# Optimization experiments

Measured on AMD Instinct MI355X. Metric: run time of the kernel, lower is better.

## Reference

```python
import jax, jax.numpy as jnp
import numpy as np

N_HEADS = 16


def setup_inputs() -> dict:
    key = jax.random.key(0)
    ks = jax.random.split(key, 9)
    B, T, C, S = 32, 8, 1024, 4096
    w_scale = 1.0 / np.sqrt(C).astype(np.float32)
    return {
        "x": jax.random.normal(ks[0], (B, T, C), jnp.float32),
        "cache_k": jax.random.normal(ks[1], (B, S, C), jnp.float32),
        "cache_v": jax.random.normal(ks[2], (B, S, C), jnp.float32),
        "cache_len": jax.random.randint(ks[3], (B,), 0, S - T, jnp.int32),
        "wq": jax.random.normal(ks[4], (C, C), jnp.float32) * w_scale,
        "wk": jax.random.normal(ks[5], (C, C), jnp.float32) * w_scale,
        "wv": jax.random.normal(ks[6], (C, C), jnp.float32) * w_scale,
        "wo": jax.random.normal(ks[7], (C, C), jnp.float32) * w_scale,
        "bo": jnp.zeros((C,), jnp.float32),
    }


def reference(x, cache_k, cache_v, cache_len, wq, wk, wv, wo, bo):
    # Decode step with KV cache (use_cache=True, window_size=None, mask=None).
    B, T, C = x.shape
    S = cache_k.shape[1]  # max_seq_len (static pad; torch pads to max(cache_len))
    H = N_HEADS
    hd = C // H

    # Projections (torch Linear: y = x @ W^T)
    q = x @ wq.T
    k_new = x @ wk.T
    v_new = x @ wv.T

    # Ragged past-KV gather: zero-pad each row beyond its cache_len,
    # exactly like the per-batch loop + padded_k/padded_v in torch.
    pos = jnp.arange(S)
    past_mask = (pos[None, :] < cache_len[:, None])[..., None]  # (B, S, 1)
    past_k = jnp.where(past_mask, cache_k, 0.0)
    past_v = jnp.where(past_mask, cache_v, 0.0)

    k = jnp.concatenate([past_k, k_new], axis=1)  # (B, S+T, C)
    v = jnp.concatenate([past_v, v_new], axis=1)

    def to_heads(t):
        return t.reshape(B, t.shape[1], H, hd).transpose(0, 2, 1, 3)

    qh, kh, vh = to_heads(q), to_heads(k), to_heads(v)  # (B,H,*,hd)

    scores = jnp.einsum('bhqd,bhkd->bhqk', qh, kh) / np.sqrt(hd).astype(np.float32)

    # Torch only materializes keys up to max(cache_len); slots beyond that
    # do not exist there, so mask them out. Slots in [cache_len_b, max_cl)
    # are zero-padded keys (score 0, value 0) in torch -> kept as-is here.
    max_cl = jnp.max(cache_len)
    key_valid = jnp.concatenate([pos < max_cl, jnp.ones((T,), bool)])  # (S+T,)
    NEG = jnp.float32(-1e30)
    scores = jnp.where(key_valid[None, None, None, :], scores, NEG)

    attn = jax.nn.softmax(scores, axis=-1)
    out = jnp.einsum('bhqk,bhkd->bhqd', attn, vh)
    out = out.transpose(0, 2, 1, 3).reshape(B, T, C)
    return out @ wo.T + bo
```

## Files before the change

### kernel.cpp

```cpp
#include <hip/hip_runtime.h>

constexpr int Bn = 32, Tn = 8, Cn = 1024, Sn = 4096, Hn = 16, HDn = 64;
constexpr int CHUNK = 64, NCHUNK = 64;
constexpr int KSPLIT = 4;
constexpr float SCALE = 0.125f;

constexpr size_t PROJ_PART = (size_t)Bn * Tn * Cn;
constexpr size_t QP_OFF = 0;
constexpr size_t KP_OFF = QP_OFF + KSPLIT * PROJ_PART;
constexpr size_t VP_OFF = KP_OFF + KSPLIT * PROJ_PART;
constexpr size_t PACC_OFF = VP_OFF + KSPLIT * PROJ_PART;
constexpr size_t PACC_SZ = (size_t)NCHUNK * Bn * Hn * Tn * HDn;
constexpr size_t PL_OFF = PACC_OFF + PACC_SZ;
constexpr size_t PL_SZ = (size_t)NCHUNK * Bn * Hn * Tn;
constexpr size_t AW_OFF = PL_OFF + PL_SZ;
constexpr size_t AW_SZ = PROJ_PART;
constexpr size_t OP_OFF = AW_OFF + AW_SZ;
constexpr size_t OP_SZ = (size_t)KSPLIT * PROJ_PART;
constexpr size_t QR_OFF = OP_OFF + OP_SZ;
constexpr size_t KN_OFF = QR_OFF + PROJ_PART;
constexpr size_t VN_OFF = KN_OFF + PROJ_PART;

typedef __attribute__((address_space(3))) unsigned int lds_uint;
typedef const __attribute__((address_space(1))) unsigned int glb_uint;

__device__ __forceinline__ void gload_lds16(const float* g, float* l) {
    __builtin_amdgcn_global_load_lds((glb_uint*)g, (lds_uint*)l, 16, 0, 0);
}

__device__ __forceinline__ void gemm_body(const float* __restrict__ X,
                                          const float* __restrict__ W,
                                          float* __restrict__ Opart,
                                          int sigma, int jblk, int iblk) {
    __shared__ float wl[64][68];
    const int tid = threadIdx.x;
    const int c = tid & 15, a = tid >> 4;
    const int j0 = jblk * 64;
    const int ib = iblk * 64 + a * 4;
    const int k0 = sigma * 256;

    float acc[4][4];
#pragma unroll
    for (int ii = 0; ii < 4; ++ii)
#pragma unroll
        for (int jj = 0; jj < 4; ++jj) acc[ii][jj] = 0.f;

    for (int kt = 0; kt < 4; ++kt) {
        const int k1 = k0 + kt * 64;
#pragma unroll
        for (int stp = 0; stp < 4; ++stp) {
            int f4 = stp * 256 + tid;
            int jr = f4 >> 4, e4 = f4 & 15;
            float4 wv = *(const float4*)&W[(size_t)(j0 + jr) * Cn + k1 + e4 * 4];
            wl[e4 * 4 + 0][jr] = wv.x;
            wl[e4 * 4 + 1][jr] = wv.y;
            wl[e4 * 4 + 2][jr] = wv.z;
            wl[e4 * 4 + 3][jr] = wv.w;
        }
        __syncthreads();
#pragma unroll 4
        for (int k4 = 0; k4 < 16; ++k4) {
            float4 xv[4];
#pragma unroll
            for (int ii = 0; ii < 4; ++ii)
                xv[ii] = *(const float4*)&X[(size_t)(ib + ii) * Cn + k1 + k4 * 4];
#pragma unroll
            for (int kk = 0; kk < 4; ++kk) {
                float4 wv = *(const float4*)&wl[k4 * 4 + kk][c * 4];
#pragma unroll
                for (int ii = 0; ii < 4; ++ii) {
                    const float xs = (kk == 0) ? xv[ii].x : (kk == 1) ? xv[ii].y
                                   : (kk == 2) ? xv[ii].z : xv[ii].w;
                    acc[ii][0] += xs * wv.x;
                    acc[ii][1] += xs * wv.y;
                    acc[ii][2] += xs * wv.z;
                    acc[ii][3] += xs * wv.w;
                }
            }
        }
        __syncthreads();
    }
    float* op = Opart + (size_t)sigma * PROJ_PART;
#pragma unroll
    for (int ii = 0; ii < 4; ++ii) {
        float4 o = make_float4(acc[ii][0], acc[ii][1], acc[ii][2], acc[ii][3]);
        *(float4*)&op[(size_t)(ib + ii) * Cn + j0 + c * 4] = o;
    }
}

__global__ __launch_bounds__(256) void proj3_kernel(
    const float* __restrict__ X, const float* __restrict__ W0,
    const float* __restrict__ W1, const float* __restrict__ W2,
    float* __restrict__ O0, float* __restrict__ O1, float* __restrict__ O2) {
    const int z = blockIdx.z;
    const float* W = (z < 4) ? W0 : (z < 8 ? W1 : W2);
    float* O = (z < 4) ? O0 : (z < 8 ? O1 : O2);
    gemm_body(X, W, O, z & 3, blockIdx.x, blockIdx.y);
}

__global__ __launch_bounds__(256) void gemm1_kernel(
    const float* __restrict__ X, const float* __restrict__ W, float* __restrict__ O) {
    gemm_body(X, W, O, blockIdx.z, blockIdx.x, blockIdx.y);
}

__global__ __launch_bounds__(256) void prereduce_kernel(
    const float* __restrict__ qp, const float* __restrict__ kp,
    const float* __restrict__ vp, float* __restrict__ q,
    float* __restrict__ kn, float* __restrict__ vn) {
    const size_t i = ((size_t)blockIdx.x * 256 + threadIdx.x) * 4;
#define SUM4(P)                                                              \
    make_float4(                                                             \
        (*(const float4*)(P + i)).x + (*(const float4*)(P + PROJ_PART + i)).x + \
        (*(const float4*)(P + 2 * PROJ_PART + i)).x + (*(const float4*)(P + 3 * PROJ_PART + i)).x, \
        (*(const float4*)(P + i)).y + (*(const float4*)(P + PROJ_PART + i)).y + \
        (*(const float4*)(P + 2 * PROJ_PART + i)).y + (*(const float4*)(P + 3 * PROJ_PART + i)).y, \
        (*(const float4*)(P + i)).z + (*(const float4*)(P + PROJ_PART + i)).z + \
        (*(const float4*)(P + 2 * PROJ_PART + i)).z + (*(const float4*)(P + 3 * PROJ_PART + i)).z, \
        (*(const float4*)(P + i)).w + (*(const float4*)(P + PROJ_PART + i)).w + \
        (*(const float4*)(P + 2 * PROJ_PART + i)).w + (*(const float4*)(P + 3 * PROJ_PART + i)).w)
    float4 qv = SUM4(qp);
    qv.x *= SCALE; qv.y *= SCALE; qv.z *= SCALE; qv.w *= SCALE;
    *(float4*)&q[i] = qv;
    *(float4*)&kn[i] = SUM4(kp);
    *(float4*)&vn[i] = SUM4(vp);
#undef SUM4
}

__global__ __launch_bounds__(64) void attn_kernel(
    const float* __restrict__ q, const float* __restrict__ kn,
    const float* __restrict__ vn, const float* __restrict__ ck,
    const float* __restrict__ cv, const int* __restrict__ clen,
    float* __restrict__ pacc, float* __restrict__ pl) {
    const int h = blockIdx.x, cq = blockIdx.y, b = blockIdx.z;
    const int cl = clen[b];
    if (cq != 0 && cq * CHUNK >= cl) return;

    const int lane = threadIdx.x;
    const int rg = lane >> 4;
    const int slot = lane & 15;

    __shared__ float K_l[64][64];
    __shared__ float V_l[64][64];
    __shared__ float q_l[8][64];
    __shared__ float p_l[8][64];

    {
        const float* qb = q + (size_t)b * Tn * Cn + (size_t)h * HDn;
#pragma unroll
        for (int i = 0; i < 2; ++i) {
            const int row = i * 4 + rg;
            gload_lds16(qb + (size_t)row * Cn + slot * 4, &q_l[i * 4][0]);
        }
    }
    const size_t gb = ((size_t)b * Sn + (size_t)cq * CHUNK) * Cn + (size_t)h * HDn;
#pragma unroll
    for (int i = 0; i < 16; ++i) {
        const int row = i * 4 + rg;
        gload_lds16(ck + gb + (size_t)row * Cn + (slot ^ (row & 15)) * 4, &K_l[i * 4][0]);
    }
#pragma unroll
    for (int i = 0; i < 16; ++i) {
        const int row = i * 4 + rg;
        gload_lds16(cv + gb + (size_t)row * Cn + slot * 4, &V_l[i * 4][0]);
    }

    int mv = clen[lane & 31];
#pragma unroll
    for (int off = 16; off >= 1; off >>= 1) {
        int o = __shfl_xor(mv, off);
        mv = mv > o ? mv : o;
    }

    const int nv = min(max(cl - cq * CHUNK, 0), CHUNK);

    asm volatile("s_waitcnt vmcnt(0)" ::: "memory");
    __builtin_amdgcn_sched_barrier(0);

    float s[8];
#pragma unroll
    for (int t = 0; t < 8; ++t) s[t] = 0.f;
    const int swz = lane & 15;
#pragma unroll
    for (int dg = 0; dg < 16; ++dg) {
        const float4 kv = *(const float4*)&K_l[lane][(dg ^ swz) * 4];
#pragma unroll
        for (int t = 0; t < 8; ++t) {
            const float4 qv = *(const float4*)&q_l[t][dg * 4];
            s[t] += kv.x * qv.x + kv.y * qv.y + kv.z * qv.z + kv.w * qv.w;
        }
    }
    const bool val = lane < nv;
    float lden[8];
#pragma unroll
    for (int t = 0; t < 8; ++t) {
        const float p = val ? __expf(s[t]) : 0.f;
        lden[t] = p;
        p_l[t][lane] = p;
    }

    float av[8];
#pragma unroll
    for (int t = 0; t < 8; ++t) av[t] = 0.f;
#pragma unroll 4
    for (int r4 = 0; r4 < 16; ++r4) {
        float4 pt[8];
#pragma unroll
        for (int t = 0; t < 8; ++t) pt[t] = *(const float4*)&p_l[t][r4 * 4];
        const float v0 = V_l[r4 * 4 + 0][lane];
        const float v1 = V_l[r4 * 4 + 1][lane];
        const float v2 = V_l[r4 * 4 + 2][lane];
        const float v3 = V_l[r4 * 4 + 3][lane];
#pragma unroll
        for (int t = 0; t < 8; ++t)
            av[t] += pt[t].x * v0 + pt[t].y * v1 + pt[t].z * v2 + pt[t].w * v3;
    }

    if (cq == 0) {
        const int r = lane >> 3, dgrp = lane & 7;
        const float* kb = kn + ((size_t)b * Tn + r) * Cn + (size_t)h * HDn + dgrp * 8;
        const float4 ka = *(const float4*)(kb);
        const float4 kc = *(const float4*)(kb + 4);
        float sn[8];
#pragma unroll
        for (int t = 0; t < 8; ++t) {
            const float4 qa = *(const float4*)&q_l[t][dgrp * 8];
            const float4 qc = *(const float4*)&q_l[t][dgrp * 8 + 4];
            float v = ka.x * qa.x + ka.y * qa.y + ka.z * qa.z + ka.w * qa.w +
                      kc.x * qc.x + kc.y * qc.y + kc.z * qc.z + kc.w * qc.w;
            v += __shfl_xor(v, 1);
            v += __shfl_xor(v, 2);
            v += __shfl_xor(v, 4);
            sn[t] = v;
        }
        if (dgrp == 0) {
#pragma unroll
            for (int t = 0; t < 8; ++t) {
                const float p = __expf(sn[t]);
                p_l[t][r] = p;
                lden[t] += p;
            }
        }
        const float* vb2 = vn + (size_t)b * Tn * Cn + (size_t)h * HDn + lane;
#pragma unroll
        for (int r2 = 0; r2 < 8; ++r2) {
            const float v = vb2[(size_t)r2 * Cn];
#pragma unroll
            for (int t = 0; t < 8; ++t) av[t] += p_l[t][r2] * v;
        }
    }

#pragma unroll
    for (int t = 0; t < 8; ++t) {
        float v = lden[t];
#pragma unroll
        for (int off = 32; off >= 1; off >>= 1) v += __shfl_xor(v, off);
        lden[t] = v;
    }
    if (cq == 0) {
        const float pad = (float)(mv - cl);
#pragma unroll
        for (int t = 0; t < 8; ++t) lden[t] += pad;
    }

    const size_t obase = (size_t)((cq * Bn + b) * Hn + h);
#pragma unroll
    for (int t = 0; t < 8; ++t) pacc[obase * 512 + (size_t)t * 64 + lane] = av[t];
    if (lane == 0) {
#pragma unroll
        for (int t = 0; t < 8; ++t) pl[obase * 8 + t] = lden[t];
    }
}

__global__ __launch_bounds__(256) void attn_merge_kernel(
    const float* __restrict__ pacc, const float* __restrict__ pl,
    const int* __restrict__ clen, float* __restrict__ aw) {
    const int h = blockIdx.x, b = blockIdx.y;
    const int tid = threadIdx.x, wave = tid >> 6, lane = tid & 63;
    const int cl = clen[b];
    int nch = (cl + CHUNK - 1) / CHUNK;
    if (nch < 1) nch = 1;

    __shared__ float racc[4][8][64];
    __shared__ float rl[4][8];

    float acc[8], l[8];
#pragma unroll
    for (int t = 0; t < 8; ++t) { acc[t] = 0.f; l[t] = 0.f; }
    for (int c = wave; c < nch; c += 4) {
        const size_t base = (size_t)((c * Bn + b) * Hn + h);
#pragma unroll
        for (int t = 0; t < 8; ++t) acc[t] += pacc[base * 512 + t * 64 + lane];
#pragma unroll
        for (int t = 0; t < 8; ++t) l[t] += pl[base * 8 + t];
    }
#pragma unroll
    for (int t = 0; t < 8; ++t) racc[wave][t][lane] = acc[t];
    if (lane == 0) {
#pragma unroll
        for (int t = 0; t < 8; ++t) rl[wave][t] = l[t];
    }
    __syncthreads();
#pragma unroll
    for (int rep = 0; rep < 2; ++rep) {
        const int e = rep * 256 + tid;
        const int t = e >> 6, d = e & 63;
        const float a = racc[0][t][d] + racc[1][t][d] + racc[2][t][d] + racc[3][t][d];
        const float ll = rl[0][t] + rl[1][t] + rl[2][t] + rl[3][t];
        aw[(size_t)(b * Tn + t) * Cn + (size_t)h * HDn + d] = a / ll;
    }
}

__global__ __launch_bounds__(256) void bias_out_kernel(
    const float* __restrict__ opart, const float* __restrict__ bo, float* __restrict__ out) {
    const int f4 = blockIdx.x * 256 + threadIdx.x;
    const float4 a0 = *(const float4*)(opart + (size_t)f4 * 4);
    const float4 a1 = *(const float4*)(opart + PROJ_PART + (size_t)f4 * 4);
    const float4 a2 = *(const float4*)(opart + 2 * PROJ_PART + (size_t)f4 * 4);
    const float4 a3 = *(const float4*)(opart + 3 * PROJ_PART + (size_t)f4 * 4);
    const float4 bv = *(const float4*)&bo[(f4 & 255) * 4];
    float4 o = make_float4(a0.x + a1.x + a2.x + a3.x + bv.x,
                           a0.y + a1.y + a2.y + a3.y + bv.y,
                           a0.z + a1.z + a2.z + a3.z + bv.z,
                           a0.w + a1.w + a2.w + a3.w + bv.w);
    *(float4*)&out[(size_t)f4 * 4] = o;
}

extern "C" void kernel_launch(void* const* d_in, const int* in_sizes, int n_in,
                              void* d_out, int out_size, void* d_ws, size_t ws_size,
                              hipStream_t stream) {
    const float* x  = (const float*)d_in[0];
    const float* ck = (const float*)d_in[1];
    const float* cv = (const float*)d_in[2];
    const int*   cl = (const int*)d_in[3];
    const float* wq = (const float*)d_in[4];
    const float* wk = (const float*)d_in[5];
    const float* wv = (const float*)d_in[6];
    const float* wo = (const float*)d_in[7];
    const float* bo = (const float*)d_in[8];
    float* out = (float*)d_out;
    float* ws = (float*)d_ws;

    float* qpart = ws + QP_OFF;
    float* kpart = ws + KP_OFF;
    float* vpart = ws + VP_OFF;
    float* pacc  = ws + PACC_OFF;
    float* pl    = ws + PL_OFF;
    float* aw    = ws + AW_OFF;
    float* opart = ws + OP_OFF;
    float* qr    = ws + QR_OFF;
    float* knew  = ws + KN_OFF;
    float* vnew  = ws + VN_OFF;

    proj3_kernel<<<dim3(16, 4, 12), dim3(256), 0, stream>>>(x, wq, wk, wv, qpart, kpart, vpart);
    prereduce_kernel<<<dim3(256), dim3(256), 0, stream>>>(qpart, kpart, vpart, qr, knew, vnew);
    attn_kernel<<<dim3(Hn, NCHUNK, Bn), dim3(64), 0, stream>>>(qr, knew, vnew, ck, cv, cl, pacc, pl);
    attn_merge_kernel<<<dim3(Hn, Bn), dim3(256), 0, stream>>>(pacc, pl, cl, aw);
    gemm1_kernel<<<dim3(16, 4, KSPLIT), dim3(256), 0, stream>>>(aw, wo, opart);
    bias_out_kernel<<<dim3(256), dim3(256), 0, stream>>>(opart, bo, out);
}
```

Before: 223.8 us.

## Make attention kernel persistent and stream V rows through registers

The attention kernel becomes a persistent grid of 2048 single-wave blocks that grid-stride over (batch, chunk, head) work items instead of launching one block per item. V is no longer staged in LDS; it is loaded into registers in four 16-row groups, with each next group's loads issued before the P·V accumulation of the current group so they overlap. Q is read directly from global memory (cache) instead of LDS, and a partial vmcnt wait lets the QK step start once K has landed. This cuts LDS use and per-block launch cost and hides V latency, at the cost of more registers, repeated global Q reads, and possible load imbalance from the fixed strided work split.

Measured after the change: 320.8 us. 1.43x slower.

```diff
diff --git a/kernel.cpp b/kernel.cpp
--- a/kernel.cpp
+++ b/kernel.cpp
@@ -2,6 +2,7 @@
 
 constexpr int Bn = 32, Tn = 8, Cn = 1024, Sn = 4096, Hn = 16, HDn = 64;
 constexpr int CHUNK = 64, NCHUNK = 64;
+constexpr int PERSIST = 2048;
 constexpr int KSPLIT = 4;
 constexpr float SCALE = 0.125f;
 
@@ -131,38 +132,13 @@
     const float* __restrict__ vn, const float* __restrict__ ck,
     const float* __restrict__ cv, const int* __restrict__ clen,
     float* __restrict__ pacc, float* __restrict__ pl) {
-    const int h = blockIdx.x, cq = blockIdx.y, b = blockIdx.z;
-    const int cl = clen[b];
-    if (cq != 0 && cq * CHUNK >= cl) return;
-
     const int lane = threadIdx.x;
     const int rg = lane >> 4;
     const int slot = lane & 15;
+    const int swz = lane & 15;
 
     __shared__ float K_l[64][64];
-    __shared__ float V_l[64][64];
-    __shared__ float q_l[8][64];
     __shared__ float p_l[8][64];
-
-    {
-        const float* qb = q + (size_t)b * Tn * Cn + (size_t)h * HDn;
-#pragma unroll
-        for (int i = 0; i < 2; ++i) {
-            const int row = i * 4 + rg;
-            gload_lds16(qb + (size_t)row * Cn + slot * 4, &q_l[i * 4][0]);
-        }
-    }
-    const size_t gb = ((size_t)b * Sn + (size_t)cq * CHUNK) * Cn + (size_t)h * HDn;
-#pragma unroll
-    for (int i = 0; i < 16; ++i) {
-        const int row = i * 4 + rg;
-        gload_lds16(ck + gb + (size_t)row * Cn + (slot ^ (row & 15)) * 4, &K_l[i * 4][0]);
-    }
-#pragma unroll
-    for (int i = 0; i < 16; ++i) {
-        const int row = i * 4 + rg;
-        gload_lds16(cv + gb + (size_t)row * Cn + slot * 4, &V_l[i * 4][0]);
-    }
 
     int mv = clen[lane & 31];
 #pragma unroll
@@ -171,103 +147,147 @@
         mv = mv > o ? mv : o;
     }
 
-    const int nv = min(max(cl - cq * CHUNK, 0), CHUNK);
-
-    asm volatile("s_waitcnt vmcnt(0)" ::: "memory");
-    __builtin_amdgcn_sched_barrier(0);
-
-    float s[8];
-#pragma unroll
-    for (int t = 0; t < 8; ++t) s[t] = 0.f;
-    const int swz = lane & 15;
-#pragma unroll
-    for (int dg = 0; dg < 16; ++dg) {
-        const float4 kv = *(const float4*)&K_l[lane][(dg ^ swz) * 4];
+    const int nItems = Bn * Hn * NCHUNK;
+    for (int widx = blockIdx.x; widx < nItems; widx += PERSIST) {
+        const int h = widx & (Hn - 1);
+        const int bc = widx >> 4;
+        const int cq = bc & (NCHUNK - 1);
+        const int b = bc >> 6;
+        const int cl = clen[b];
+        if (cq != 0 && cq * CHUNK >= cl) continue;
+        const int nv = min(max(cl - cq * CHUNK, 0), CHUNK);
+
+        const size_t gb = ((size_t)b * Sn + (size_t)cq * CHUNK) * Cn + (size_t)h * HDn;
+#pragma unroll
+        for (int i = 0; i < 16; ++i) {
+            const int row = i * 4 + rg;
+            gload_lds16(ck + gb + (size_t)row * Cn + (slot ^ (row & 15)) * 4, &K_l[i * 4][0]);
+        }
+        const float* vb = cv + gb + lane;
+        float vq0[16];
+#pragma unroll
+        for (int r = 0; r < 16; ++r) vq0[r] = vb[(size_t)r * Cn];
+
+        asm volatile("s_waitcnt vmcnt(16)" ::: "memory");
+        __builtin_amdgcn_sched_barrier(0);
+
+        const float* qb = q + (size_t)b * Tn * Cn + (size_t)h * HDn;
+        float s[8];
+#pragma unroll
+        for (int t = 0; t < 8; ++t) s[t] = 0.f;
+#pragma unroll
+        for (int dg = 0; dg < 16; ++dg) {
+            const float4 kv = *(const float4*)&K_l[lane][(dg ^ swz) * 4];
+#pragma unroll
+            for (int t = 0; t < 8; ++t) {
+                const float4 qv = *(const float4*)(qb + (size_t)t * Cn + dg * 4);
+                s[t] += kv.x * qv.x + kv.y * qv.y + kv.z * qv.z + kv.w * qv.w;
+            }
+        }
+        const bool val = lane < nv;
+        float lden[8];
 #pragma unroll
         for (int t = 0; t < 8; ++t) {
-            const float4 qv = *(const float4*)&q_l[t][dg * 4];
-            s[t] += kv.x * qv.x + kv.y * qv.y + kv.z * qv.z + kv.w * qv.w;
-        }
-    }
-    const bool val = lane < nv;
-    float lden[8];
-#pragma unroll
-    for (int t = 0; t < 8; ++t) {
-        const float p = val ? __expf(s[t]) : 0.f;
-        lden[t] = p;
-        p_l[t][lane] = p;
-    }
-
-    float av[8];
-#pragma unroll
-    for (int t = 0; t < 8; ++t) av[t] = 0.f;
-#pragma unroll 4
-    for (int r4 = 0; r4 < 16; ++r4) {
-        float4 pt[8];
-#pragma unroll
-        for (int t = 0; t < 8; ++t) pt[t] = *(const float4*)&p_l[t][r4 * 4];
-        const float v0 = V_l[r4 * 4 + 0][lane];
-        const float v1 = V_l[r4 * 4 + 1][lane];
-        const float v2 = V_l[r4 * 4 + 2][lane];
-        const float v3 = V_l[r4 * 4 + 3][lane];
-#pragma unroll
-        for (int t = 0; t < 8; ++t)
-            av[t] += pt[t].x * v0 + pt[t].y * v1 + pt[t].z * v2 + pt[t].w * v3;
-    }
-
-    if (cq == 0) {
-        const int r = lane >> 3, dgrp = lane & 7;
-        const float* kb = kn + ((size_t)b * Tn + r) * Cn + (size_t)h * HDn + dgrp * 8;
-        const float4 ka = *(const float4*)(kb);
-        const float4 kc = *(const float4*)(kb + 4);
-        float sn[8];
+            const float p = val ? __expf(s[t]) : 0.f;
+            lden[t] = p;
+            p_l[t][lane] = p;
+        }
+
+        float av[8];
+#pragma unroll
+        for (int t = 0; t < 8; ++t) av[t] = 0.f;
+
+#define PVQ(VQ, BASE)                                                         \
+    do {                                                                      \
+        _Pragma("unroll")                                                     \
+        for (int r4 = 0; r4 < 4; ++r4) {                                      \
+            float4 pt[8];                                                     \
+            _Pragma("unroll")                                                 \
+            for (int t = 0; t < 8; ++t)                                       \
+                pt[t] = *(const float4*)&p_l[t][(BASE) + r4 * 4];             \
+            _Pragma("unroll")                                                 \
+            for (int u = 0; u < 4; ++u) {                                     \
+                const float v = VQ[r4 * 4 + u];                               \
+                _Pragma("unroll")                                             \
+                for (int t = 0; t < 8; ++t) {                                 \
+                    const float pu = (u == 0) ? pt[t].x                       \
+                                   : (u == 1) ? pt[t].y                       \
+                                   : (u == 2) ? pt[t].z : pt[t].w;            \
+                    av[t] += pu * v;                                          \
+                }                                                             \
+            }                                                                 \
+        }                                                                     \
+    } while (0)
+
+        float vq1[16];
+#pragma unroll
+        for (int r = 0; r < 16; ++r) vq1[r] = vb[(size_t)(16 + r) * Cn];
+        PVQ(vq0, 0);
+        float vq2[16];
+#pragma unroll
+        for (int r = 0; r < 16; ++r) vq2[r] = vb[(size_t)(32 + r) * Cn];
+        PVQ(vq1, 16);
+        float vq3[16];
+#pragma unroll
+        for (int r = 0; r < 16; ++r) vq3[r] = vb[(size_t)(48 + r) * Cn];
+        PVQ(vq2, 32);
+        PVQ(vq3, 48);
+#undef PVQ
+
+        if (cq == 0) {
+            const int r = lane >> 3, dgrp = lane & 7;
+            const float* kb = kn + ((size_t)b * Tn + r) * Cn + (size_t)h * HDn + dgrp * 8;
+            const float4 ka = *(const float4*)(kb);
+            const float4 kc = *(const float4*)(kb + 4);
+            float sn[8];
+#pragma unroll
+            for (int t = 0; t < 8; ++t) {
+                const float4 qa = *(const float4*)(qb + (size_t)t * Cn + dgrp * 8);
+                const float4 qc = *(const float4*)(qb + (size_t)t * Cn + dgrp * 8 + 4);
+                float v = ka.x * qa.x + ka.y * qa.y + ka.z * qa.z + ka.w * qa.w +
+                          kc.x * qc.x + kc.y * qc.y + kc.z * qc.z + kc.w * qc.w;
+                v += __shfl_xor(v, 1);
+                v += __shfl_xor(v, 2);
+                v += __shfl_xor(v, 4);
+                sn[t] = v;
+            }
+            if (dgrp == 0) {
+#pragma unroll
+                for (int t = 0; t < 8; ++t) {
+                    const float p = __expf(sn[t]);
+                    p_l[t][r] = p;
+                    lden[t] += p;
+                }
+            }
+            const float* vb2 = vn + (size_t)b * Tn * Cn + (size_t)h * HDn + lane;
+#pragma unroll
+            for (int r2 = 0; r2 < 8; ++r2) {
+                const float v = vb2[(size_t)r2 * Cn];
+#pragma unroll
+                for (int t = 0; t < 8; ++t) av[t] += p_l[t][r2] * v;
+            }
+        }
+
 #pragma unroll
         for (int t = 0; t < 8; ++t) {
-            const float4 qa = *(const float4*)&q_l[t][dgrp * 8];
-            const float4 qc = *(const float4*)&q_l[t][dgrp * 8 + 4];
-            float v = ka.x * qa.x + ka.y * qa.y + ka.z * qa.z + ka.w * qa.w +
-                      kc.x * qc.x + kc.y * qc.y + kc.z * qc.z + kc.w * qc.w;
-            v += __shfl_xor(v, 1);
-            v += __shfl_xor(v, 2);
-            v += __shfl_xor(v, 4);
-            sn[t] = v;
-        }
-        if (dgrp == 0) {
-#pragma unroll
-            for (int t = 0; t < 8; ++t) {
-                const float p = __expf(sn[t]);
-                p_l[t][r] = p;
-                lden[t] += p;
-            }
-        }
-        const float* vb2 = vn + (size_t)b * Tn * Cn + (size_t)h * HDn + lane;
-#pragma unroll
-        for (int r2 = 0; r2 < 8; ++r2) {
-            const float v = vb2[(size_t)r2 * Cn];
-#pragma unroll
-            for (int t = 0; t < 8; ++t) av[t] += p_l[t][r2] * v;
-        }
-    }
-
-#pragma unroll
-    for (int t = 0; t < 8; ++t) {
-        float v = lden[t];
-#pragma unroll
-        for (int off = 32; off >= 1; off >>= 1) v += __shfl_xor(v, off);
-        lden[t] = v;
-    }
-    if (cq == 0) {
-        const float pad = (float)(mv - cl);
-#pragma unroll
-        for (int t = 0; t < 8; ++t) lden[t] += pad;
-    }
-
-    const size_t obase = (size_t)((cq * Bn + b) * Hn + h);
-#pragma unroll
-    for (int t = 0; t < 8; ++t) pacc[obase * 512 + (size_t)t * 64 + lane] = av[t];
-    if (lane == 0) {
-#pragma unroll
-        for (int t = 0; t < 8; ++t) pl[obase * 8 + t] = lden[t];
+            float v = lden[t];
+#pragma unroll
+            for (int off = 32; off >= 1; off >>= 1) v += __shfl_xor(v, off);
+            lden[t] = v;
+        }
+        if (cq == 0) {
+            const float pad = (float)(mv - cl);
+#pragma unroll
+            for (int t = 0; t < 8; ++t) lden[t] += pad;
+        }
+
+        const size_t obase = (size_t)((cq * Bn + b) * Hn + h);
+#pragma unroll
+        for (int t = 0; t < 8; ++t) pacc[obase * 512 + (size_t)t * 64 + lane] = av[t];
+        if (lane == 0) {
+#pragma unroll
+            for (int t = 0; t < 8; ++t) pl[obase * 8 + t] = lden[t];
+        }
     }
 }
 
@@ -353,7 +373,7 @@
 
     proj3_kernel<<<dim3(16, 4, 12), dim3(256), 0, stream>>>(x, wq, wk, wv, qpart, kpart, vpart);
     prereduce_kernel<<<dim3(256), dim3(256), 0, stream>>>(qpart, kpart, vpart, qr, knew, vnew);
-    attn_kernel<<<dim3(Hn, NCHUNK, Bn), dim3(64), 0, stream>>>(qr, knew, vnew, ck, cv, cl, pacc, pl);
+    attn_kernel<<<dim3(PERSIST), dim3(64), 0, stream>>>(qr, knew, vnew, ck, cv, cl, pacc, pl);
     attn_merge_kernel<<<dim3(Hn, Bn), dim3(256), 0, stream>>>(pacc, pl, cl, aw);
     gemm1_kernel<<<dim3(16, 4, KSPLIT), dim3(256), 0, stream>>>(aw, wo, opart);
     bias_out_kernel<<<dim3(256), dim3(256), 0, stream>>>(opart, bo, out);
```

## Restructure attention kernel to process four heads per wave with double-buffered KV streaming

Applied to the files above, without the earlier changes.

Each 64-lane block now covers four heads (256 contiguous channels) of a 64-row chunk instead of one head. It streams K in 16-row sub-steps through LDS, and loads V straight into registers with double buffering so the next step's loads overlap the current compute. This aims to give wider contiguous 1KB row reads, cut the block count by four, and hide memory latency. The costs are much higher register pressure from two 16-entry float4 V buffers plus 32 accumulators, and fewer blocks in flight to hide latency.

Result: no change. 224.0 us (+0.1%).

```diff
diff --git a/kernel.cpp b/kernel.cpp
--- a/kernel.cpp
+++ b/kernel.cpp
@@ -126,43 +126,22 @@
 #undef SUM4
 }
 
-__global__ __launch_bounds__(64) void attn_kernel(
+__global__ __launch_bounds__(64, 1) void attn_kernel(
     const float* __restrict__ q, const float* __restrict__ kn,
     const float* __restrict__ vn, const float* __restrict__ ck,
     const float* __restrict__ cv, const int* __restrict__ clen,
     float* __restrict__ pacc, float* __restrict__ pl) {
-    const int h = blockIdx.x, cq = blockIdx.y, b = blockIdx.z;
+    const int hq = blockIdx.x, CQ = blockIdx.y, b = blockIdx.z;
     const int cl = clen[b];
-    if (cq != 0 && cq * CHUNK >= cl) return;
+    if (CQ != 0 && CQ * CHUNK >= cl) return;
 
     const int lane = threadIdx.x;
-    const int rg = lane >> 4;
-    const int slot = lane & 15;
-
-    __shared__ float K_l[64][64];
-    __shared__ float V_l[64][64];
-    __shared__ float q_l[8][64];
+    const int h4 = lane >> 4;
+    const int c4 = lane & 15;
+
+    __shared__ float K_l[16][256];
+    __shared__ float q_l[8][256];
     __shared__ float p_l[8][64];
-
-    {
-        const float* qb = q + (size_t)b * Tn * Cn + (size_t)h * HDn;
-#pragma unroll
-        for (int i = 0; i < 2; ++i) {
-            const int row = i * 4 + rg;
-            gload_lds16(qb + (size_t)row * Cn + slot * 4, &q_l[i * 4][0]);
-        }
-    }
-    const size_t gb = ((size_t)b * Sn + (size_t)cq * CHUNK) * Cn + (size_t)h * HDn;
-#pragma unroll
-    for (int i = 0; i < 16; ++i) {
-        const int row = i * 4 + rg;
-        gload_lds16(ck + gb + (size_t)row * Cn + (slot ^ (row & 15)) * 4, &K_l[i * 4][0]);
-    }
-#pragma unroll
-    for (int i = 0; i < 16; ++i) {
-        const int row = i * 4 + rg;
-        gload_lds16(cv + gb + (size_t)row * Cn + slot * 4, &V_l[i * 4][0]);
-    }
 
     int mv = clen[lane & 31];
 #pragma unroll
@@ -171,101 +150,189 @@
         mv = mv > o ? mv : o;
     }
 
-    const int nv = min(max(cl - cq * CHUNK, 0), CHUNK);
-
-    asm volatile("s_waitcnt vmcnt(0)" ::: "memory");
+    {
+        const float* qb = q + (size_t)b * Tn * Cn + hq * 256;
+#pragma unroll
+        for (int t = 0; t < 8; ++t)
+            gload_lds16(qb + (size_t)t * Cn + lane * 4, &q_l[t][0]);
+    }
     __builtin_amdgcn_sched_barrier(0);
 
-    float s[8];
-#pragma unroll
-    for (int t = 0; t < 8; ++t) s[t] = 0.f;
-    const int swz = lane & 15;
-#pragma unroll
-    for (int dg = 0; dg < 16; ++dg) {
-        const float4 kv = *(const float4*)&K_l[lane][(dg ^ swz) * 4];
+    const int nv = min(max(cl - CQ * CHUNK, 0), CHUNK);
+    const int nst = (nv + 15) >> 4;
+
+    const size_t kvbase = ((size_t)b * Sn + (size_t)CQ * CHUNK) * Cn + hq * 256;
+    const float* kbase = ck + kvbase;
+    const float* vbase = cv + kvbase;
+
+    float av[8][4];
+#pragma unroll
+    for (int t = 0; t < 8; ++t) av[t][0] = av[t][1] = av[t][2] = av[t][3] = 0.f;
+    float lden[8];
+#pragma unroll
+    for (int t = 0; t < 8; ++t) lden[t] = 0.f;
+
+    auto issueK = [&](int s) {
+#pragma unroll
+        for (int i = 0; i < 16; ++i) {
+            const int sslot = (lane & 48) | ((lane & 15) ^ i);
+            gload_lds16(kbase + (size_t)(s * 16 + i) * Cn + sslot * 4, &K_l[i][0]);
+        }
+    };
+    auto issueV = [&](int s, float4 (&vr)[16]) {
+#pragma unroll
+        for (int i = 0; i < 16; ++i)
+            vr[i] = *(const float4*)(vbase + (size_t)(s * 16 + i) * Cn + lane * 4);
+    };
+    auto doQK = [&](int s) {
+        float sc[8];
+#pragma unroll
+        for (int t = 0; t < 8; ++t) sc[t] = 0.f;
+#pragma unroll
+        for (int dg = 0; dg < 16; ++dg) {
+            const float4 kv = *(const float4*)&K_l[c4][(h4 * 16 + (dg ^ c4)) * 4];
+#pragma unroll
+            for (int t = 0; t < 8; ++t) {
+                const float4 qv = *(const float4*)&q_l[t][h4 * 64 + dg * 4];
+                sc[t] += kv.x * qv.x + kv.y * qv.y + kv.z * qv.z + kv.w * qv.w;
+            }
+        }
+        const bool val = (s * 16 + c4) < nv;
 #pragma unroll
         for (int t = 0; t < 8; ++t) {
-            const float4 qv = *(const float4*)&q_l[t][dg * 4];
-            s[t] += kv.x * qv.x + kv.y * qv.y + kv.z * qv.z + kv.w * qv.w;
-        }
-    }
-    const bool val = lane < nv;
-    float lden[8];
-#pragma unroll
-    for (int t = 0; t < 8; ++t) {
-        const float p = val ? __expf(s[t]) : 0.f;
-        lden[t] = p;
-        p_l[t][lane] = p;
-    }
-
-    float av[8];
-#pragma unroll
-    for (int t = 0; t < 8; ++t) av[t] = 0.f;
-#pragma unroll 4
-    for (int r4 = 0; r4 < 16; ++r4) {
-        float4 pt[8];
-#pragma unroll
-        for (int t = 0; t < 8; ++t) pt[t] = *(const float4*)&p_l[t][r4 * 4];
-        const float v0 = V_l[r4 * 4 + 0][lane];
-        const float v1 = V_l[r4 * 4 + 1][lane];
-        const float v2 = V_l[r4 * 4 + 2][lane];
-        const float v3 = V_l[r4 * 4 + 3][lane];
-#pragma unroll
-        for (int t = 0; t < 8; ++t)
-            av[t] += pt[t].x * v0 + pt[t].y * v1 + pt[t].z * v2 + pt[t].w * v3;
-    }
-
-    if (cq == 0) {
-        const int r = lane >> 3, dgrp = lane & 7;
-        const float* kb = kn + ((size_t)b * Tn + r) * Cn + (size_t)h * HDn + dgrp * 8;
-        const float4 ka = *(const float4*)(kb);
-        const float4 kc = *(const float4*)(kb + 4);
-        float sn[8];
-#pragma unroll
-        for (int t = 0; t < 8; ++t) {
-            const float4 qa = *(const float4*)&q_l[t][dgrp * 8];
-            const float4 qc = *(const float4*)&q_l[t][dgrp * 8 + 4];
-            float v = ka.x * qa.x + ka.y * qa.y + ka.z * qa.z + ka.w * qa.w +
-                      kc.x * qc.x + kc.y * qc.y + kc.z * qc.z + kc.w * qc.w;
-            v += __shfl_xor(v, 1);
-            v += __shfl_xor(v, 2);
-            v += __shfl_xor(v, 4);
-            sn[t] = v;
-        }
-        if (dgrp == 0) {
+            const float p = val ? __expf(sc[t]) : 0.f;
+            lden[t] += p;
+            p_l[t][lane] = p;
+        }
+    };
+    auto doPV = [&](float4 (&vr)[16]) {
+#pragma unroll
+        for (int r4 = 0; r4 < 4; ++r4) {
+            float4 pt[8];
+#pragma unroll
+            for (int t = 0; t < 8; ++t) pt[t] = *(const float4*)&p_l[t][h4 * 16 + r4 * 4];
+#pragma unroll
+            for (int u = 0; u < 4; ++u) {
+                const float4 vv = vr[r4 * 4 + u];
+#pragma unroll
+                for (int t = 0; t < 8; ++t) {
+                    const float pu = (u == 0) ? pt[t].x : (u == 1) ? pt[t].y
+                                   : (u == 2) ? pt[t].z : pt[t].w;
+                    av[t][0] += pu * vv.x;
+                    av[t][1] += pu * vv.y;
+                    av[t][2] += pu * vv.z;
+                    av[t][3] += pu * vv.w;
+                }
+            }
+        }
+    };
+
+    if (nst > 0) {
+        float4 vA[16], vB[16];
+        issueK(0);
+        __builtin_amdgcn_sched_barrier(0);
+        issueV(0, vA);
+        __builtin_amdgcn_sched_barrier(0);
+        int s = 0;
+        for (;;) {
+            asm volatile("s_waitcnt vmcnt(16)" ::: "memory");
+            __builtin_amdgcn_sched_barrier(0);
+            doQK(s);
+            asm volatile("s_waitcnt lgkmcnt(0)" ::: "memory");
+            __builtin_amdgcn_sched_barrier(0);
+            if (s + 1 < nst) {
+                issueK(s + 1);
+                __builtin_amdgcn_sched_barrier(0);
+                issueV(s + 1, vB);
+                __builtin_amdgcn_sched_barrier(0);
+            }
+            doPV(vA);
+            if (++s >= nst) break;
+            asm volatile("s_waitcnt vmcnt(16)" ::: "memory");
+            __builtin_amdgcn_sched_barrier(0);
+            doQK(s);
+            asm volatile("s_waitcnt lgkmcnt(0)" ::: "memory");
+            __builtin_amdgcn_sched_barrier(0);
+            if (s + 1 < nst) {
+                issueK(s + 1);
+                __builtin_amdgcn_sched_barrier(0);
+                issueV(s + 1, vA);
+                __builtin_amdgcn_sched_barrier(0);
+            }
+            doPV(vB);
+            if (++s >= nst) break;
+        }
+    }
+
+    if (CQ == 0) {
+        if (lane < 32) {
+            const int hN = lane >> 3, rN = lane & 7;
+            const float* kb2 = kn + ((size_t)b * Tn + rN) * Cn + hq * 256 + hN * 64;
+            float sd[8];
+#pragma unroll
+            for (int t = 0; t < 8; ++t) sd[t] = 0.f;
+#pragma unroll
+            for (int j = 0; j < 16; ++j) {
+                const float4 kf = *(const float4*)(kb2 + j * 4);
+#pragma unroll
+                for (int t = 0; t < 8; ++t) {
+                    const float4 qf = *(const float4*)&q_l[t][hN * 64 + j * 4];
+                    sd[t] += kf.x * qf.x + kf.y * qf.y + kf.z * qf.z + kf.w * qf.w;
+                }
+            }
+#pragma unroll
+            for (int t = 0; t < 8; ++t) p_l[t][hN * 16 + rN] = __expf(sd[t]);
+        }
+        asm volatile("s_waitcnt lgkmcnt(0)" ::: "memory");
+        __builtin_amdgcn_sched_barrier(0);
+#pragma unroll
+        for (int r4 = 0; r4 < 2; ++r4) {
+            float4 pt[8];
+#pragma unroll
+            for (int t = 0; t < 8; ++t) pt[t] = *(const float4*)&p_l[t][h4 * 16 + r4 * 4];
+#pragma unroll
+            for (int u = 0; u < 4; ++u) {
+                const int r = r4 * 4 + u;
+                const float4 vv = *(const float4*)(vn + ((size_t)b * Tn + r) * Cn +
+                                                   hq * 256 + h4 * 64 + c4 * 4);
+#pragma unroll
+                for (int t = 0; t < 8; ++t) {
+                    const float pu = (u == 0) ? pt[t].x : (u == 1) ? pt[t].y
+                                   : (u == 2) ? pt[t].z : pt[t].w;
+                    av[t][0] += pu * vv.x;
+                    av[t][1] += pu * vv.y;
+                    av[t][2] += pu * vv.z;
+                    av[t][3] += pu * vv.w;
+                }
+            }
+        }
+        if (c4 == 0) {
 #pragma unroll
             for (int t = 0; t < 8; ++t) {
-                const float p = __expf(sn[t]);
-                p_l[t][r] = p;
-                lden[t] += p;
-            }
-        }
-        const float* vb2 = vn + (size_t)b * Tn * Cn + (size_t)h * HDn + lane;
-#pragma unroll
-        for (int r2 = 0; r2 < 8; ++r2) {
-            const float v = vb2[(size_t)r2 * Cn];
-#pragma unroll
-            for (int t = 0; t < 8; ++t) av[t] += p_l[t][r2] * v;
+                float ss = 0.f;
+#pragma unroll
+                for (int r = 0; r < 8; ++r) ss += p_l[t][h4 * 16 + r];
+                lden[t] += ss + (float)(mv - cl);
+            }
         }
     }
 
 #pragma unroll
     for (int t = 0; t < 8; ++t) {
         float v = lden[t];
-#pragma unroll
-        for (int off = 32; off >= 1; off >>= 1) v += __shfl_xor(v, off);
+        v += __shfl_xor(v, 1);
+        v += __shfl_xor(v, 2);
+        v += __shfl_xor(v, 4);
+        v += __shfl_xor(v, 8);
         lden[t] = v;
     }
-    if (cq == 0) {
-        const float pad = (float)(mv - cl);
-#pragma unroll
-        for (int t = 0; t < 8; ++t) lden[t] += pad;
-    }
-
-    const size_t obase = (size_t)((cq * Bn + b) * Hn + h);
-#pragma unroll
-    for (int t = 0; t < 8; ++t) pacc[obase * 512 + (size_t)t * 64 + lane] = av[t];
-    if (lane == 0) {
+
+    const size_t obase = (size_t)((CQ * Bn + b) * Hn + hq * 4 + h4);
+#pragma unroll
+    for (int t = 0; t < 8; ++t)
+        *(float4*)&pacc[obase * 512 + (size_t)t * 64 + c4 * 4] =
+            make_float4(av[t][0], av[t][1], av[t][2], av[t][3]);
+    if (c4 == 0) {
 #pragma unroll
         for (int t = 0; t < 8; ++t) pl[obase * 8 + t] = lden[t];
     }
@@ -353,7 +420,7 @@
 
     proj3_kernel<<<dim3(16, 4, 12), dim3(256), 0, stream>>>(x, wq, wk, wv, qpart, kpart, vpart);
     prereduce_kernel<<<dim3(256), dim3(256), 0, stream>>>(qpart, kpart, vpart, qr, knew, vnew);
-    attn_kernel<<<dim3(Hn, NCHUNK, Bn), dim3(64), 0, stream>>>(qr, knew, vnew, ck, cv, cl, pacc, pl);
+    attn_kernel<<<dim3(4, NCHUNK, Bn), dim3(64), 0, stream>>>(qr, knew, vnew, ck, cv, cl, pacc, pl);
     attn_merge_kernel<<<dim3(Hn, Bn), dim3(256), 0, stream>>>(pacc, pl, cl, aw);
     gemm1_kernel<<<dim3(16, 4, KSPLIT), dim3(256), 0, stream>>>(aw, wo, opart);
     bias_out_kernel<<<dim3(256), dim3(256), 0, stream>>>(opart, bo, out);
```
